# Optimization experiments

Measured on AMD Instinct MI355X. Metric: run time of the kernel, lower is better.

## Reference

```python
import jax, jax.numpy as jnp
import numpy as np

K = 5  # per_pix_kernel


def spatial_attention(x, w):
    # x: [N, k^2, H, W]; w: [1, 2, 7, 7] conv weight, padding=3, no bias
    avg = jnp.mean(x, axis=1, keepdims=True)
    mx = jnp.max(x, axis=1, keepdims=True)
    s = jnp.concatenate([avg, mx], axis=1)  # [N,2,H,W]
    y = jax.lax.conv_general_dilated(
        s, w, window_strides=(1, 1), padding=[(3, 3), (3, 3)],
        dimension_numbers=('NCHW', 'OIHW', 'NCHW'))
    return jax.nn.sigmoid(y)  # [N,1,H,W]


def fac(feat, filters, k):
    # feat: [N,C,H,W]; filters: [N,k^2,H,W] per-pixel kernel shared across channels
    N, C, H, W = feat.shape
    pad = (k - 1) // 2
    p = jnp.pad(feat, ((0, 0), (0, 0), (pad, pad), (pad, pad)))
    # patches[n,c,h,w,s] with s = kh*k + kw (matches torch unfold(2).unfold(3) row-major order)
    patches = jnp.stack([p[:, :, i:i + H, j:j + W]
                         for i in range(k) for j in range(k)], axis=-1)
    return jnp.einsum('nchws,nshw->nchw', patches, filters)


def setup_inputs() -> dict:
    key = jax.random.key(0)
    ks = jax.random.split(key, 7)
    N, C, H, W = 16, 3, 256, 256
    return {
        'blur_info': jax.random.normal(ks[0], (N, C, H, W), jnp.float32),
        'perpix_1': jax.random.normal(ks[1], (N, K * K, H, W), jnp.float32),
        'perpix_2': jax.random.normal(ks[2], (N, K * K, H, W), jnp.float32),
        'perpix_3': jax.random.normal(ks[3], (N, K * K, H, W), jnp.float32),
        'w1': jax.random.normal(ks[4], (1, 2, 7, 7), jnp.float32) * 0.1,
        'w2': jax.random.normal(ks[5], (1, 2, 7, 7), jnp.float32) * 0.1,
        'w3': jax.random.normal(ks[6], (1, 2, 7, 7), jnp.float32) * 0.1,
    }


def reference(blur_info, perpix_1, perpix_2, perpix_3, w1, w2, w3):
    perpix = [perpix_1, perpix_2, perpix_3]
    weights = [w1, w2, w3]
    reblur = []
    for pk, w in zip(perpix, weights):
        mask = spatial_attention(pk, w)            # [N,1,H,W]
        sharp = blur_info * (1.0 - mask)
        blur = fac(blur_info * mask, pk, K)        # per-pixel adaptive filtering
        reblur.append(sharp + blur)
    out = reblur[0]
    for r in reblur[1:]:
        out = out + r
    return out / len(reblur)
```

## Files before the change

### kernel.cpp

```cpp
#include <hip/hip_runtime.h>

#define NIMG 16
#define NC 3
#define H 256
#define W 256
#define HW (H * W)
#define NS 25
#define TH 16
#define TW 16
#define SRH (TH + 10)
#define SRW (TW + 10)
#define SRN (SRH * SRW)
#define MRH (TH + 4)
#define MRW (TW + 4)
#define MRN (MRH * MRW)
#define NTHREADS 256
#define NHALO (SRN - TH * TW)

__device__ __forceinline__ unsigned bf16r(float x) {
    union { float f; unsigned u; } c; c.f = x;
    return (c.u + 0x7FFFu + ((c.u >> 16) & 1u)) >> 16;
}
__device__ __forceinline__ float bf_hi(unsigned u) {
    union { unsigned u; float f; } c; c.u = u & 0xFFFF0000u; return c.f;
}
__device__ __forceinline__ float bf_lo(unsigned u) {
    union { unsigned u; float f; } c; c.u = u << 16; return c.f;
}

__global__ __launch_bounds__(NTHREADS, 2)
void reblur_fused(const float* __restrict__ blur_info,
                  const float* __restrict__ pp0,
                  const float* __restrict__ pp1,
                  const float* __restrict__ pp2,
                  const float* __restrict__ wt0,
                  const float* __restrict__ wt1,
                  const float* __restrict__ wt2,
                  float* __restrict__ out)
{
    __shared__ unsigned s_l[SRN];
    __shared__ float q[NC][MRN];
    __shared__ float wts[3][98];

    const int tid = threadIdx.x;

    const int id  = blockIdx.x + (blockIdx.y << 4) + (blockIdx.z << 8);
    const int sid = ((id & 7) << 9) + (id >> 3);
    const int n   = sid >> 8;
    const int h0  = ((sid >> 4) & 15) * TH;
    const int w0  = (sid & 15) * TW;

    if (tid < 98) {
        float sc = (tid < 49) ? 0.04f : 1.0f;
        wts[0][tid] = wt0[tid] * sc;
        wts[1][tid] = wt1[tid] * sc;
        wts[2][tid] = wt2[tid] * sc;
    }

    float facc0 = 0.f, facc1 = 0.f, facc2 = 0.f;

    const size_t nbase = (size_t)n * NS * HW;
    const int r = tid >> 4, c = tid & 15;

    float pk[NS];

    #pragma unroll 1
    for (int b = 0; b < 3; ++b) {
        const float* pb = (b == 0) ? pp0 : ((b == 1) ? pp1 : pp2);
        pb += nbase;

        {
            const float* p = pb + (h0 + r) * W + (w0 + c);
            float v = p[0];
            pk[0] = v;
            float sm = v, mx = v;
            #pragma unroll
            for (int s = 1; s < NS; ++s) {
                v = p[s * HW];
                pk[s] = v;
                sm += v; mx = fmaxf(mx, v);
            }
            s_l[(r + 5) * SRW + (c + 5)] = (bf16r(sm) << 16) | bf16r(mx);
        }

        for (int m = tid; m < NHALO; m += NTHREADS) {
            int rr, cc;
            if (m < 130)      { rr = m / 26;              cc = m % 26; }
            else if (m < 260) { int t = m - 130; rr = 21 + t / 26; cc = t % 26; }
            else              { int t = m - 260; rr = 5 + t / 10;
                                int c2 = t % 10; cc = (c2 < 5) ? c2 : c2 + 16; }
            const int gh = h0 - 5 + rr, gw = w0 - 5 + cc;
            unsigned u = 0;
            if ((unsigned)gh < H && (unsigned)gw < W) {
                const float* p = pb + gh * W + gw;
                float v = p[0];
                float sm = v, mx = v;
                #pragma unroll
                for (int s = 1; s < NS; ++s) {
                    v = p[s * HW];
                    sm += v; mx = fmaxf(mx, v);
                }
                u = (bf16r(sm) << 16) | bf16r(mx);
            }
            s_l[rr * SRW + cc] = u;
        }
        __syncthreads();

        const float* wb = &wts[b][0];
        for (int i = tid; i < MRN; i += NTHREADS) {
            int rr = i / MRW, cc = i % MRW;
            float a = 0.f;
            #pragma unroll
            for (int j = 0; j < 7; ++j) {
                #pragma unroll
                for (int t = 0; t < 7; ++t) {
                    unsigned u = s_l[(rr + j) * SRW + cc + t];
                    a += bf_hi(u) * wb[j * 7 + t] + bf_lo(u) * wb[49 + j * 7 + t];
                }
            }
            float m = 1.f / (1.f + __expf(-a));
            int gh = h0 - 2 + rr, gw = w0 - 2 + cc;
            bool inb = (unsigned)gh < H && (unsigned)gw < W;
            int gi = gh * W + gw;
            #pragma unroll
            for (int cch = 0; cch < NC; ++cch) {
                float bv = inb ? blur_info[(n * NC + cch) * HW + gi] : 0.f;
                q[cch][i] = m * bv;
            }
        }
        __syncthreads();

        {
            const int qc = (r + 2) * MRW + c + 2;
            float f0 = -q[0][qc], f1 = -q[1][qc], f2 = -q[2][qc];
            #pragma unroll
            for (int s = 0; s < NS; ++s) {
                const int qi = (r + s / 5) * MRW + c + (s % 5);
                const float v = pk[s];
                f0 += v * q[0][qi];
                f1 += v * q[1][qi];
                f2 += v * q[2][qi];
            }
            facc0 += f0; facc1 += f1; facc2 += f2;
        }
    }

    const float inv3 = 1.f / 3.f;
    const int gi = (h0 + r) * W + (w0 + c);
    out[(n * NC + 0) * HW + gi] = blur_info[(n * NC + 0) * HW + gi] + facc0 * inv3;
    out[(n * NC + 1) * HW + gi] = blur_info[(n * NC + 1) * HW + gi] + facc1 * inv3;
    out[(n * NC + 2) * HW + gi] = blur_info[(n * NC + 2) * HW + gi] + facc2 * inv3;
}

extern "C" void kernel_launch(void* const* d_in, const int* in_sizes, int n_in,
                              void* d_out, int out_size, void* d_ws, size_t ws_size,
                              hipStream_t stream) {
    const float* blur = (const float*)d_in[0];
    float* out = (float*)d_out;

    dim3 grid(W / TW, H / TH, NIMG);
    reblur_fused<<<grid, NTHREADS, 0, stream>>>(
        blur,
        (const float*)d_in[1], (const float*)d_in[2], (const float*)d_in[3],
        (const float*)d_in[4], (const float*)d_in[5], (const float*)d_in[6],
        out);
}
```

Before: 387.2 us.

## Store attention stats as fp32 float2, vectorize conv and FAC shared-memory reads

Replaces the bf16-packed avg/max shared tile with an fp32 float2 tile (padded row width 28) and drops the shared weight staging in favour of direct global reads of the conv weights. The 7x7 conv is restructured so each thread computes two adjacent outputs from float4 row loads, and blur_info is read as float2. The masked q values move to an interleaved float4 layout so the FAC loop does one vector LDS read per tap. This cuts bf16 packing ALU work and shared-load instruction count, at the cost of more LDS capacity and fewer active threads in the conv phase (200 of 256).

```diff
diff --git a/kernel.cpp b/kernel.cpp
--- a/kernel.cpp
+++ b/kernel.cpp
@@ -9,24 +9,15 @@
 #define TH 16
 #define TW 16
 #define SRH (TH + 10)
-#define SRW (TW + 10)
+#define SRC (TW + 10)
+#define SRW 28
 #define SRN (SRH * SRW)
 #define MRH (TH + 4)
 #define MRW (TW + 4)
 #define MRN (MRH * MRW)
+#define NPAIR (MRN / 2)
 #define NTHREADS 256
-#define NHALO (SRN - TH * TW)
-
-__device__ __forceinline__ unsigned bf16r(float x) {
-    union { float f; unsigned u; } c; c.f = x;
-    return (c.u + 0x7FFFu + ((c.u >> 16) & 1u)) >> 16;
-}
-__device__ __forceinline__ float bf_hi(unsigned u) {
-    union { unsigned u; float f; } c; c.u = u & 0xFFFF0000u; return c.f;
-}
-__device__ __forceinline__ float bf_lo(unsigned u) {
-    union { unsigned u; float f; } c; c.u = u << 16; return c.f;
-}
+#define NHALO (SRH * SRC - TH * TW)
 
 __global__ __launch_bounds__(NTHREADS, 2)
 void reblur_fused(const float* __restrict__ blur_info,
@@ -38,9 +29,8 @@
                   const float* __restrict__ wt2,
                   float* __restrict__ out)
 {
-    __shared__ unsigned s_l[SRN];
-    __shared__ float q[NC][MRN];
-    __shared__ float wts[3][98];
+    __shared__ __attribute__((aligned(16))) float2 s_l[SRN];
+    __shared__ float4 q4[MRN];
 
     const int tid = threadIdx.x;
 
@@ -49,13 +39,6 @@
     const int n   = sid >> 8;
     const int h0  = ((sid >> 4) & 15) * TH;
     const int w0  = (sid & 15) * TW;
-
-    if (tid < 98) {
-        float sc = (tid < 49) ? 0.04f : 1.0f;
-        wts[0][tid] = wt0[tid] * sc;
-        wts[1][tid] = wt1[tid] * sc;
-        wts[2][tid] = wt2[tid] * sc;
-    }
 
     float facc0 = 0.f, facc1 = 0.f, facc2 = 0.f;
 
@@ -67,6 +50,7 @@
     #pragma unroll 1
     for (int b = 0; b < 3; ++b) {
         const float* pb = (b == 0) ? pp0 : ((b == 1) ? pp1 : pp2);
+        const float* wb = (b == 0) ? wt0 : ((b == 1) ? wt1 : wt2);
         pb += nbase;
 
         {
@@ -80,7 +64,7 @@
                 pk[s] = v;
                 sm += v; mx = fmaxf(mx, v);
             }
-            s_l[(r + 5) * SRW + (c + 5)] = (bf16r(sm) << 16) | bf16r(mx);
+            s_l[(r + 5) * SRW + (c + 5)] = make_float2(sm * 0.04f, mx);
         }
 
         for (int m = tid; m < NHALO; m += NTHREADS) {
@@ -90,7 +74,7 @@
             else              { int t = m - 260; rr = 5 + t / 10;
                                 int c2 = t % 10; cc = (c2 < 5) ? c2 : c2 + 16; }
             const int gh = h0 - 5 + rr, gw = w0 - 5 + cc;
-            unsigned u = 0;
+            float2 u = make_float2(0.f, 0.f);
             if ((unsigned)gh < H && (unsigned)gw < W) {
                 const float* p = pb + gh * W + gw;
                 float v = p[0];
@@ -100,46 +84,61 @@
                     v = p[s * HW];
                     sm += v; mx = fmaxf(mx, v);
                 }
-                u = (bf16r(sm) << 16) | bf16r(mx);
+                u = make_float2(sm * 0.04f, mx);
             }
             s_l[rr * SRW + cc] = u;
         }
         __syncthreads();
 
-        const float* wb = &wts[b][0];
-        for (int i = tid; i < MRN; i += NTHREADS) {
-            int rr = i / MRW, cc = i % MRW;
-            float a = 0.f;
+        if (tid < NPAIR) {
+            const int rr  = tid / 10;
+            const int cc0 = (tid % 10) * 2;
+            float a0 = 0.f, a1 = 0.f;
             #pragma unroll
             for (int j = 0; j < 7; ++j) {
-                #pragma unroll
-                for (int t = 0; t < 7; ++t) {
-                    unsigned u = s_l[(rr + j) * SRW + cc + t];
-                    a += bf_hi(u) * wb[j * 7 + t] + bf_lo(u) * wb[49 + j * 7 + t];
-                }
+                const float4* rw =
+                    reinterpret_cast<const float4*>(s_l + (rr + j) * SRW + cc0);
+                float4 t0 = rw[0], t1 = rw[1], t2 = rw[2], t3 = rw[3];
+                const float* waj = wb + j * 7;
+                const float* wmj = wb + 49 + j * 7;
+                a0 += t0.x*waj[0] + t0.y*wmj[0] + t0.z*waj[1] + t0.w*wmj[1]
+                    + t1.x*waj[2] + t1.y*wmj[2] + t1.z*waj[3] + t1.w*wmj[3]
+                    + t2.x*waj[4] + t2.y*wmj[4] + t2.z*waj[5] + t2.w*wmj[5]
+                    + t3.x*waj[6] + t3.y*wmj[6];
+                a1 += t0.z*waj[0] + t0.w*wmj[0]
+                    + t1.x*waj[1] + t1.y*wmj[1] + t1.z*waj[2] + t1.w*wmj[2]
+                    + t2.x*waj[3] + t2.y*wmj[3] + t2.z*waj[4] + t2.w*wmj[4]
+                    + t3.x*waj[5] + t3.y*wmj[5] + t3.z*waj[6] + t3.w*wmj[6];
             }
-            float m = 1.f / (1.f + __expf(-a));
-            int gh = h0 - 2 + rr, gw = w0 - 2 + cc;
-            bool inb = (unsigned)gh < H && (unsigned)gw < W;
-            int gi = gh * W + gw;
-            #pragma unroll
-            for (int cch = 0; cch < NC; ++cch) {
-                float bv = inb ? blur_info[(n * NC + cch) * HW + gi] : 0.f;
-                q[cch][i] = m * bv;
+            const float m0 = 1.f / (1.f + __expf(-a0));
+            const float m1 = 1.f / (1.f + __expf(-a1));
+            const int gh  = h0 - 2 + rr;
+            const int gw0 = w0 - 2 + cc0;
+            const bool inb = ((unsigned)gh < H) && ((unsigned)gw0 < W);
+            const int gi = gh * W + gw0;
+            float2 b0 = make_float2(0.f, 0.f), b1 = b0, b2 = b0;
+            if (inb) {
+                b0 = *reinterpret_cast<const float2*>(&blur_info[(n * NC + 0) * HW + gi]);
+                b1 = *reinterpret_cast<const float2*>(&blur_info[(n * NC + 1) * HW + gi]);
+                b2 = *reinterpret_cast<const float2*>(&blur_info[(n * NC + 2) * HW + gi]);
             }
+            const int qi = rr * MRW + cc0;
+            q4[qi]     = make_float4(m0 * b0.x, m0 * b1.x, m0 * b2.x, 0.f);
+            q4[qi + 1] = make_float4(m1 * b0.y, m1 * b1.y, m1 * b2.y, 0.f);
         }
         __syncthreads();
 
         {
-            const int qc = (r + 2) * MRW + c + 2;
-            float f0 = -q[0][qc], f1 = -q[1][qc], f2 = -q[2][qc];
+            const float4* qb = q4 + r * MRW + c;
+            const float4 Qc = qb[2 * MRW + 2];
+            float f0 = -Qc.x, f1 = -Qc.y, f2 = -Qc.z;
             #pragma unroll
             for (int s = 0; s < NS; ++s) {
-                const int qi = (r + s / 5) * MRW + c + (s % 5);
+                const float4 Q = qb[(s / 5) * MRW + (s % 5)];
                 const float v = pk[s];
-                f0 += v * q[0][qi];
-                f1 += v * q[1][qi];
-                f2 += v * q[2][qi];
+                f0 += v * Q.x;
+                f1 += v * Q.y;
+                f2 += v * Q.z;
             }
             facc0 += f0; facc1 += f1; facc2 += f2;
         }
```

Result: slower. 395.5 us (+2.1%).
